# Performance work log

Measured on AMD Instinct MI355X. Metric: run time of the kernel, lower is better.

Reference implementation:

```python
import jax, jax.numpy as jnp
import numpy as np

# LLaMA-style decoder config (shrunken for reference): L layers, hidden D, H heads,
# SwiGLU width F, vocab V, LoRA rank R.
B, S, D, H, F, V, L, R = 2, 512, 1024, 16, 4096, 32000, 2, 16
DH = D // H
LORA_ALPHA = 32.0
EPS = 1e-5
ROPE_THETA = 10000.0


def setup_inputs() -> dict:
    key = jax.random.key(0)
    ks = iter(jax.random.split(key, 40))
    def n(shape, std=0.02):
        return jax.random.normal(next(ks), shape, jnp.float32) * std
    return {
        "input_ids": jax.random.randint(next(ks), (B, S), 0, V),
        "attention_mask": jnp.ones((B, S), jnp.int32),
        "embed": n((V, D)),
        "ln1": jnp.ones((L, D), jnp.float32),
        "ln2": jnp.ones((L, D), jnp.float32),
        "wq": n((L, D, D)), "aq": n((L, D, R)), "bq": n((L, R, D), 0.01),
        "wk": n((L, D, D)), "ak": n((L, D, R)), "bk": n((L, R, D), 0.01),
        "wv": n((L, D, D)), "av": n((L, D, R)), "bv": n((L, R, D), 0.01),
        "wo": n((L, D, D)), "ao": n((L, D, R)), "bo": n((L, R, D), 0.01),
        "wg": n((L, D, F)), "ag": n((L, D, R)), "bg": n((L, R, F), 0.01),
        "wu": n((L, D, F)), "au": n((L, D, R)), "bu": n((L, R, F), 0.01),
        "wd": n((L, F, D)), "ad": n((L, F, R)), "bd": n((L, R, D), 0.01),
        "final_ln": jnp.ones((D,), jnp.float32),
        "lm_head_w": n((D, V)),
        "value_w": n((D, 1)),
        "value_b": jnp.zeros((1,), jnp.float32),
    }


def _rmsnorm(x, w):
    return x * jax.lax.rsqrt(jnp.mean(x * x, axis=-1, keepdims=True) + EPS) * w


def _lin_lora(x, w, a, b):
    # base matmul + low-rank LoRA update scaled by alpha/r (dropout=eval/off)
    return x @ w + ((x @ a) @ b) * (LORA_ALPHA / R)


def _rope_cache(seq_len):
    half = DH // 2
    inv = 1.0 / (ROPE_THETA ** (jnp.arange(half, dtype=jnp.float32) / half))
    ang = jnp.arange(seq_len, dtype=jnp.float32)[:, None] * inv  # [S, half]
    ang = jnp.concatenate([ang, ang], axis=-1)                   # [S, DH]
    return jnp.cos(ang), jnp.sin(ang)


def _apply_rope(x, cos, sin):  # x: [B,S,H,DH]
    h = DH // 2
    rot = jnp.concatenate([-x[..., h:], x[..., :h]], axis=-1)
    return x * cos[None, :, None, :] + rot * sin[None, :, None, :]


def reference(input_ids, attention_mask, embed, ln1, ln2,
              wq, aq, bq, wk, ak, bk, wv, av, bv, wo, ao, bo,
              wg, ag, bg, wu, au, bu, wd, ad, bd,
              final_ln, lm_head_w, value_w, value_b):
    h = embed[input_ids]  # [B,S,D]
    cos, sin = _rope_cache(S)
    causal = jnp.tril(jnp.ones((S, S), bool))
    keep = causal[None, None, :, :] & (attention_mask[:, None, None, :] > 0)
    bias = jnp.where(keep, 0.0, -1e9)  # [B,1,S,S]
    scale = 1.0 / jnp.sqrt(jnp.float32(DH))

    for i in range(L):
        # --- self-attention block ---
        x = _rmsnorm(h, ln1[i])
        q = _lin_lora(x, wq[i], aq[i], bq[i]).reshape(B, S, H, DH)
        k = _lin_lora(x, wk[i], ak[i], bk[i]).reshape(B, S, H, DH)
        v = _lin_lora(x, wv[i], av[i], bv[i]).reshape(B, S, H, DH)
        q = _apply_rope(q, cos, sin)
        k = _apply_rope(k, cos, sin)
        scores = jnp.einsum("bqhd,bkhd->bhqk", q, k) * scale + bias
        attn = jax.nn.softmax(scores, axis=-1)
        o = jnp.einsum("bhqk,bkhd->bqhd", attn, v).reshape(B, S, D)
        h = h + _lin_lora(o, wo[i], ao[i], bo[i])
        # --- SwiGLU MLP block ---
        x = _rmsnorm(h, ln2[i])
        g = jax.nn.silu(_lin_lora(x, wg[i], ag[i], bg[i]))
        u = _lin_lora(x, wu[i], au[i], bu[i])
        h = h + _lin_lora(g * u, wd[i], ad[i], bd[i])

    h = _rmsnorm(h, final_ln)          # HF hidden_states[-1] is post final norm
    logits = h @ lm_head_w             # [B,S,V]
    values = (h @ value_w)[..., 0] + value_b[0]  # [B,S] (squeeze(-1))
    return logits, values
```

## Files before the change

### kernel.cpp

```cpp
#include <hip/hip_runtime.h>
#include <math.h>

constexpr int B = 2, S = 512, D = 1024, H = 16, F = 4096, V = 32000, L = 2, R = 16, DH = 64;
constexpr int BS = B * S;
constexpr float LORA_SCALE = 2.0f;
constexpr float EPS = 1e-5f;
constexpr int RS_QKV = 3 * D;
constexpr int RS_GU  = 2 * F;

typedef __attribute__((ext_vector_type(8))) __bf16 bf16x8;
typedef __attribute__((ext_vector_type(4))) float f32x4;

__device__ __forceinline__ unsigned short f2bf(float f) {
  unsigned u = __builtin_bit_cast(unsigned, f);
  unsigned r = (u + 0x7FFFu + ((u >> 16) & 1u)) >> 16;
  return (unsigned short)r;
}
__device__ __forceinline__ float bf2f(unsigned short us) {
  return __builtin_bit_cast(float, (unsigned)us << 16);
}
__device__ __forceinline__ void load_lds16(const void* g, void* l) {
  __builtin_amdgcn_global_load_lds((const __attribute__((address_space(1))) void*)g,
                                   (__attribute__((address_space(3))) void*)l, 16, 0, 0);
}

struct Ptr3 { const float* p[3]; };

__global__ void rope_cache_kernel(float* __restrict__ cosb, float* __restrict__ sinb) {
  int s = blockIdx.x, j = threadIdx.x;
  float inv = __expf(-(float)j * (9.210340371976184f / 32.0f));
  float ang = (float)s * inv;
  float c = cosf(ang), sn = sinf(ang);
  cosb[s * DH + j] = c;  cosb[s * DH + j + 32] = c;
  sinb[s * DH + j] = sn; sinb[s * DH + j + 32] = sn;
}

__global__ void embed_kernel(const int* __restrict__ ids, const float* __restrict__ emb,
                             float* __restrict__ h) {
  int row = blockIdx.x, t = threadIdx.x;
  int id = ids[row];
  ((float4*)(h + (size_t)row * D))[t] = ((const float4*)(emb + (size_t)id * D))[t];
}

__global__ void rmsnorm_value_kernel(const float* __restrict__ x, const float* __restrict__ w,
                                     const float* __restrict__ vw, const float* __restrict__ vb,
                                     unsigned short* __restrict__ y, float* __restrict__ values) {
  int row = blockIdx.x, t = threadIdx.x;
  int lane = t & 63;
  __shared__ float redw[4];
  __shared__ float redv[4];
  float4 xv = ((const float4*)(x + (size_t)row * D))[t];
  float ss = xv.x * xv.x + xv.y * xv.y + xv.z * xv.z + xv.w * xv.w;
#pragma unroll
  for (int off = 1; off < 64; off <<= 1) ss += __shfl_xor(ss, off);
  if (lane == 0) redw[t >> 6] = ss;
  __syncthreads();
  float rinv = rsqrtf((redw[0] + redw[1] + redw[2] + redw[3]) * (1.0f / D) + EPS);
  float4 wv = ((const float4*)w)[t];
  float4 nx;
  nx.x = xv.x * rinv * wv.x; nx.y = xv.y * rinv * wv.y;
  nx.z = xv.z * rinv * wv.z; nx.w = xv.w * rinv * wv.w;
  ushort4 o;
  o.x = f2bf(nx.x); o.y = f2bf(nx.y); o.z = f2bf(nx.z); o.w = f2bf(nx.w);
  ((ushort4*)(y + (size_t)row * D))[t] = o;
  float4 vv = ((const float4*)vw)[t];
  float vd = nx.x * vv.x + nx.y * vv.y + nx.z * vv.z + nx.w * vv.w;
#pragma unroll
  for (int off = 1; off < 64; off <<= 1) vd += __shfl_xor(vd, off);
  if (lane == 0) redv[t >> 6] = vd;
  __syncthreads();
  if (t == 0) values[row] = redv[0] + redv[1] + redv[2] + redv[3] + vb[0];
}

template <int NA>
__global__ void rms_lora_kernel(const float* __restrict__ hp, const float* __restrict__ w,
                                Ptr3 ap, unsigned short* __restrict__ xbf,
                                unsigned short* __restrict__ t2e) {
  int row = blockIdx.x, t = threadIdx.x;
  int lane = t & 63;
  __shared__ float xs[D];
  __shared__ float red[256];
  __shared__ float redw[4];
  float4 xv = ((const float4*)(hp + (size_t)row * D))[t];
  float ss = xv.x * xv.x + xv.y * xv.y + xv.z * xv.z + xv.w * xv.w;
#pragma unroll
  for (int off = 1; off < 64; off <<= 1) ss += __shfl_xor(ss, off);
  if (lane == 0) redw[t >> 6] = ss;
  __syncthreads();
  float rinv = rsqrtf((redw[0] + redw[1] + redw[2] + redw[3]) * (1.0f / D) + EPS);
  float4 wv = ((const float4*)w)[t];
  float4 nx;
  nx.x = xv.x * rinv * wv.x; nx.y = xv.y * rinv * wv.y;
  nx.z = xv.z * rinv * wv.z; nx.w = xv.w * rinv * wv.w;
  xs[t * 4 + 0] = nx.x; xs[t * 4 + 1] = nx.y; xs[t * 4 + 2] = nx.z; xs[t * 4 + 3] = nx.w;
  ushort4 o;
  o.x = f2bf(nx.x); o.y = f2bf(nx.y); o.z = f2bf(nx.z); o.w = f2bf(nx.w);
  ((ushort4*)(xbf + (size_t)row * D))[t] = o;
  if (t >= NA * 16 && t < 64) t2e[(size_t)row * 64 + t] = 0;
  __syncthreads();
  int n = t & 15, g = t >> 4;
#pragma unroll
  for (int ad = 0; ad < NA; ++ad) {
    const float* a = ap.p[ad];
    float s = 0.0f;
    for (int k = g; k < D; k += 16) s = fmaf(xs[k], a[k * 16 + n], s);
    s += __shfl_xor(s, 16);
    s += __shfl_xor(s, 32);
    if (lane < 16) red[(t >> 6) * 16 + n] = s;
    __syncthreads();
    if (t < 16) t2e[(size_t)row * 64 + ad * 16 + t] =
        f2bf(LORA_SCALE * (red[t] + red[t + 16] + red[t + 32] + red[t + 48]));
    if (ad + 1 < NA) __syncthreads();
  }
}

__global__ void lora_o_kernel(const unsigned short* __restrict__ xb, const float* __restrict__ a,
                              unsigned short* __restrict__ t2e) {
  int row = blockIdx.x, t = threadIdx.x;
  int lane = t & 63;
  __shared__ float xs[D];
  __shared__ float red[64];
  for (int k = t; k < D; k += 256) xs[k] = bf2f(xb[(size_t)row * D + k]);
  if (t >= 16 && t < 64) t2e[(size_t)row * 64 + t] = 0;
  __syncthreads();
  int n = t & 15, g = t >> 4;
  float s = 0.0f;
  for (int k = g; k < D; k += 16) s = fmaf(xs[k], a[k * 16 + n], s);
  s += __shfl_xor(s, 16);
  s += __shfl_xor(s, 32);
  if (lane < 16) red[(t >> 6) * 16 + n] = s;
  __syncthreads();
  if (t < 16) t2e[(size_t)row * 64 + t] =
      f2bf(LORA_SCALE * (red[t] + red[t + 16] + red[t + 32] + red[t + 48]));
}

__global__ void silu_lora_kernel(const unsigned short* __restrict__ gub, const float* __restrict__ a,
                                 unsigned short* __restrict__ gbf, unsigned short* __restrict__ t2e) {
  int row = blockIdx.x, t = threadIdx.x;
  int lane = t & 63;
  __shared__ float xs[F];
  __shared__ float red[64];
#pragma unroll
  for (int i2 = 0; i2 < 2; ++i2) {
    int idx = i2 * 256 + t;
    uint4 gv = ((const uint4*)(gub + (size_t)row * RS_GU))[idx];
    uint4 uv = ((const uint4*)(gub + (size_t)row * RS_GU + F))[idx];
    const unsigned* gw = (const unsigned*)&gv;
    const unsigned* uw = (const unsigned*)&uv;
    unsigned short go[8];
#pragma unroll
    for (int q = 0; q < 4; ++q) {
      float g0 = bf2f((unsigned short)(gw[q] & 0xffff)), g1 = bf2f((unsigned short)(gw[q] >> 16));
      float u0 = bf2f((unsigned short)(uw[q] & 0xffff)), u1 = bf2f((unsigned short)(uw[q] >> 16));
      float r0 = g0 / (1.0f + __expf(-g0)) * u0;
      float r1 = g1 / (1.0f + __expf(-g1)) * u1;
      xs[idx * 8 + q * 2] = r0; xs[idx * 8 + q * 2 + 1] = r1;
      go[q * 2] = f2bf(r0); go[q * 2 + 1] = f2bf(r1);
    }
    *(uint4*)(gbf + (size_t)row * F + idx * 8) = *(const uint4*)go;
  }
  if (t >= 16 && t < 64) t2e[(size_t)row * 64 + t] = 0;
  __syncthreads();
  int n = t & 15, g = t >> 4;
  float s = 0.0f;
  for (int k = g; k < F; k += 16) s = fmaf(xs[k], a[k * 16 + n], s);
  s += __shfl_xor(s, 16);
  s += __shfl_xor(s, 32);
  if (lane < 16) red[(t >> 6) * 16 + n] = s;
  __syncthreads();
  if (t < 16) t2e[(size_t)row * 64 + t] =
      f2bf(LORA_SCALE * (red[t] + red[t + 16] + red[t + 32] + red[t + 48]));
}

struct BD { const float* p0; const float* p1; const float* p2;
            unsigned short* dst; int NA; int logW; int nelem; };
struct BDs { BD d[8]; };
__global__ void bext_many_kernel(BDs da) {
  int gid = blockIdx.x * 256 + threadIdx.x;
  int di = 0;
  while (gid >= da.d[di].nelem) { gid -= da.d[di].nelem; ++di; }
  const BD dd = da.d[di];
  int n = gid >> 6, kk = gid & 63;
  int W = 1 << dd.logW;
  int sel = n >> dd.logW;
  const float* bp = (sel == 0) ? dd.p0 : (sel == 1) ? dd.p1 : dd.p2;
  float v = 0.0f;
  if ((kk >> 4) == sel && sel < dd.NA)
    v = bp[(size_t)(kk & 15) * W + (n & (W - 1))];
  dd.dst[(size_t)n * 64 + kk] = f2bf(v);
}

struct TD { const float* src; unsigned short* dst; int K; int N; int nblk; };
struct TDs { TD d[15]; };
__global__ __launch_bounds__(256) void transpose_many_kernel(TDs da) {
  __shared__ __align__(16) float tile[128 * 128];
  int bid = blockIdx.x;
  int di = 0;
  while (bid >= da.d[di].nblk) { bid -= da.d[di].nblk; ++di; }
  const TD dd = da.d[di];
  int nbx = dd.N >> 7;
  int n0 = (bid % nbx) * 128, k0 = (bid / nbx) * 128;
  int t = threadIdx.x;
#pragma unroll
  for (int i = 0; i < 16; ++i) {
    int s = i * 256 + t;
    int k = s >> 5, cp = s & 31;
    int swz = (k + (k >> 3)) & 31;
    load_lds16(dd.src + (size_t)(k0 + k) * dd.N + n0 + (cp ^ swz) * 4, &tile[s * 4]);
  }
  asm volatile("s_waitcnt vmcnt(0)" ::: "memory");
  __builtin_amdgcn_s_barrier();
#pragma unroll
  for (int j2 = 0; j2 < 8; ++j2) {
    int flat = j2 * 256 + t;
    int n = flat >> 4, kc = flat & 15;
    int n4 = n >> 2;
    unsigned short o8[8];
#pragma unroll
    for (int q = 0; q < 8; ++q) {
      int k = kc * 8 + q;
      int swz = (k + (k >> 3)) & 31;
      o8[q] = f2bf(tile[k * 128 + ((n4 ^ swz) << 2) + (n & 3)]);
    }
    *(uint4*)(dd.dst + (size_t)(n0 + n) * dd.K + k0 + kc * 8) = *(const uint4*)o8;
  }
}

template <int BM, int BN, bool ACC, bool EXT, int OM>
__global__ __launch_bounds__(256) void gemm_bf16_kernel(
    const unsigned short* __restrict__ A, const unsigned short* __restrict__ Bt,
    void* __restrict__ Cp, int M, int N, int K,
    const unsigned short* __restrict__ Ae, const unsigned short* __restrict__ Be,
    const float* __restrict__ cosb, const float* __restrict__ sinb) {
  constexpr int WC = (BM == 64 || BN == 128) ? 2 : 1;
  constexpr int WR = 4 / WC;
  constexpr int RW = BM / WR;
  constexpr int MI = RW / 16;
  constexpr int CN = BN / WC;
  constexpr int NI = CN / 16;
  constexpr int ACH = BM / 32;
  constexpr int BCH = BN / 32;
  constexpr int NLOADS = ACH + BCH;
  __shared__ __align__(16) unsigned short As[2][BM * 64];
  __shared__ __align__(16) unsigned short Bs[2][BN * 64];
  int t = threadIdx.x;
  int lane = t & 63, wave = t >> 6;
  int wr = wave / WC, wc = wave % WC;
  int MT = gridDim.y, NT = gridDim.x;
  int nwg = MT * NT;
  int orig = blockIdx.y * NT + blockIdx.x;
  int qq = nwg >> 3, rr8 = nwg & 7;
  int xcd = orig & 7, pos = orig >> 3;
  int wg = (xcd < rr8) ? (xcd * (qq + 1) + pos) : (rr8 * (qq + 1) + (xcd - rr8) * qq + pos);
  int m0 = (wg % MT) * BM, n0 = (wg / MT) * BN;
  int fr = lane & 15, fq = lane >> 4;
  int xorv = fr & 7;
  f32x4 acc[MI][NI] = {};
  int kIters = K / 64;
  int nIters = EXT ? kIters + 1 : kIters;

  auto STAGE = [&](int it, int buf) {
    bool ext = EXT && (it == kIters);
    int k0 = it * 64;
#pragma unroll
    for (int c = 0; c < ACH; ++c) {
      int i = c * 256 + t;
      int row = i >> 3, c8 = i & 7;
      int sc = (c8 ^ (row & 7)) * 8;
      const unsigned short* src = ext ? (Ae + (size_t)(m0 + row) * 64 + sc)
                                      : (A + (size_t)(m0 + row) * K + k0 + sc);
      load_lds16(src, &As[buf][i * 8]);
    }
#pragma unroll
    for (int c = 0; c < BCH; ++c) {
      int i = c * 256 + t;
      int row = i >> 3, c8 = i & 7;
      int sc = (c8 ^ (row & 7)) * 8;
      const unsigned short* src = ext ? (Be + (size_t)(n0 + row) * 64 + sc)
                                      : (Bt + (size_t)(n0 + row) * K + k0 + sc);
      load_lds16(src, &Bs[buf][i * 8]);
    }
  };

  STAGE(0, 0);
  if (nIters > 1) STAGE(1, 1);
  int cur = 0;
  for (int it = 0; it < nIters; ++it) {
    if (it + 1 < nIters) {
      if constexpr (NLOADS == 8)      asm volatile("s_waitcnt vmcnt(8)" ::: "memory");
      else if constexpr (NLOADS == 6) asm volatile("s_waitcnt vmcnt(6)" ::: "memory");
      else                            asm volatile("s_waitcnt vmcnt(4)" ::: "memory");
    } else {
      asm volatile("s_waitcnt vmcnt(0)" ::: "memory");
    }
    __builtin_amdgcn_s_barrier();
#pragma unroll
    for (int kk = 0; kk < 2; ++kk) {
      bf16x8 af[MI], bfr[NI];
#pragma unroll
      for (int mi = 0; mi < MI; ++mi)
        af[mi] = *(const bf16x8*)(&As[cur][(wr * RW + mi * 16 + fr) * 64 + (((kk * 4 + fq) ^ xorv) << 3)]);
#pragma unroll
      for (int ni = 0; ni < NI; ++ni)
        bfr[ni] = *(const bf16x8*)(&Bs[cur][(wc * CN + ni * 16 + fr) * 64 + (((kk * 4 + fq) ^ xorv) << 3)]);
#pragma unroll
      for (int mi = 0; mi < MI; ++mi)
#pragma unroll
        for (int ni = 0; ni < NI; ++ni)
          acc[mi][ni] = __builtin_amdgcn_mfma_f32_16x16x32_bf16(af[mi], bfr[ni], acc[mi][ni], 0, 0, 0);
    }
    __builtin_amdgcn_s_barrier();
    if (it + 2 < nIters) STAGE(it + 2, cur);
    cur ^= 1;
  }
  if constexpr (OM == 0) {
    float* C = (float*)Cp;
#pragma unroll
    for (int mi = 0; mi < MI; ++mi)
#pragma unroll
      for (int ni = 0; ni < NI; ++ni)
#pragma unroll
        for (int j = 0; j < 4; ++j) {
          int r = m0 + wr * RW + mi * 16 + fq * 4 + j;
          int cl = n0 + wc * CN + ni * 16 + fr;
          size_t idx = (size_t)r * N + cl;
          float v = acc[mi][ni][j];
          C[idx] = ACC ? C[idx] + v : v;
        }
  } else {
    unsigned short* Cb = (unsigned short*)Cp;
#pragma unroll
    for (int mi = 0; mi < MI; ++mi)
#pragma unroll
      for (int j = 0; j < 4; ++j) {
        int r = m0 + wr * RW + mi * 16 + fq * 4 + j;
        if constexpr (OM == 2) {
          int s = r & (S - 1);
#pragma unroll
          for (int ni = 0; ni < 2; ++ni) {
            int cl0 = n0 + wc * CN + ni * 16 + fr;
            int cl1 = cl0 + 32;
            float x0 = acc[mi][ni][j], x1 = acc[mi][ni + 2][j];
            if (cl0 < 2 * D) {
              int dh = cl0 & 63;
              float cz = cosb[s * DH + dh], sz = sinb[s * DH + dh];
              float y0 = x0 * cz - x1 * sz;
              float y1 = x1 * cz + x0 * sz;
              x0 = y0; x1 = y1;
            }
            Cb[(size_t)r * N + cl0] = f2bf(x0);
            Cb[(size_t)r * N + cl1] = f2bf(x1);
          }
        } else {
#pragma unroll
          for (int ni = 0; ni < NI; ++ni) {
            int cl = n0 + wc * CN + ni * 16 + fr;
            Cb[(size_t)r * N + cl] = f2bf(acc[mi][ni][j]);
          }
        }
      }
  }
}

__global__ __launch_bounds__(512) void gemm256_kernel(
    const unsigned short* __restrict__ A, const unsigned short* __restrict__ Bt,
    float* __restrict__ C, int M, int N, int K) {
  __shared__ __align__(16) unsigned short As[2][256 * 64];
  __shared__ __align__(16) unsigned short Bs[2][256 * 64];
  int t = threadIdx.x;
  int lane = t & 63, wave = t >> 6;
  int wr = wave >> 2, wc = wave & 3;
  int MT = gridDim.y, NT = gridDim.x;
  int nwg = MT * NT;
  int orig = blockIdx.y * NT + blockIdx.x;
  int qq = nwg >> 3, rr8 = nwg & 7;
  int xcd = orig & 7, pos = orig >> 3;
  int wg = (xcd < rr8) ? (xcd * (qq + 1) + pos) : (rr8 * (qq + 1) + (xcd - rr8) * qq + pos);
  int m0 = (wg % MT) * 256, n0 = (wg / MT) * 256;
  int fr = lane & 15, fq = lane >> 4;
  int xorv = fr & 7;
  f32x4 acc[8][4] = {};
  int kIters = K / 64;

  auto STAGE = [&](int it, int buf) {
    int k0 = it * 64;
#pragma unroll
    for (int c = 0; c < 4; ++c) {
      int i = c * 512 + t;
      int row = i >> 3, c8 = i & 7;
      int sc = (c8 ^ (row & 7)) * 8;
      load_lds16(A + (size_t)(m0 + row) * K + k0 + sc, &As[buf][i * 8]);
    }
#pragma unroll
    for (int c = 0; c < 4; ++c) {
      int i = c * 512 + t;
      int row = i >> 3, c8 = i & 7;
      int sc = (c8 ^ (row & 7)) * 8;
      load_lds16(Bt + (size_t)(n0 + row) * K + k0 + sc, &Bs[buf][i * 8]);
    }
  };

  STAGE(0, 0);
  if (kIters > 1) STAGE(1, 1);
  int cur = 0;
  for (int it = 0; it < kIters; ++it) {
    if (it + 1 < kIters) asm volatile("s_waitcnt vmcnt(8)" ::: "memory");
    else                 asm volatile("s_waitcnt vmcnt(0)" ::: "memory");
    __builtin_amdgcn_s_barrier();
    __builtin_amdgcn_s_setprio(1);
#pragma unroll
    for (int kk = 0; kk < 2; ++kk) {
      bf16x8 af[8], bfr[4];
#pragma unroll
      for (int mi = 0; mi < 8; ++mi)
        af[mi] = *(const bf16x8*)(&As[cur][(wr * 128 + mi * 16 + fr) * 64 + (((kk * 4 + fq) ^ xorv) << 3)]);
#pragma unroll
      for (int ni = 0; ni < 4; ++ni)
        bfr[ni] = *(const bf16x8*)(&Bs[cur][(wc * 64 + ni * 16 + fr) * 64 + (((kk * 4 + fq) ^ xorv) << 3)]);
#pragma unroll
      for (int mi = 0; mi < 8; ++mi)
#pragma unroll
        for (int ni = 0; ni < 4; ++ni)
          acc[mi][ni] = __builtin_amdgcn_mfma_f32_16x16x32_bf16(af[mi], bfr[ni], acc[mi][ni], 0, 0, 0);
    }
    __builtin_amdgcn_s_setprio(0);
    __builtin_amdgcn_s_barrier();
    if (it + 2 < kIters) STAGE(it + 2, cur);
    cur ^= 1;
  }
#pragma unroll
  for (int mi = 0; mi < 8; ++mi)
#pragma unroll
    for (int ni = 0; ni < 4; ++ni)
#pragma unroll
      for (int j = 0; j < 4; ++j) {
        int r = m0 + wr * 128 + mi * 16 + fq * 4 + j;
        int cl = n0 + wc * 64 + ni * 16 + fr;
        C[(size_t)r * N + cl] = acc[mi][ni][j];
      }
}

__global__ __launch_bounds__(256) void attn_mfma_kernel(
    const unsigned short* __restrict__ qkvb, const int* __restrict__ amask,
    unsigned short* __restrict__ o) {
  __shared__ unsigned short Qs[64 * 72];
  __shared__ unsigned short Ks[64 * 72];
  __shared__ unsigned short Vt[64 * 72];
  __shared__ unsigned short Ps[4][16 * 72];
  __shared__ float msk[64];
  int bid = blockIdx.x;
  int qt = bid & 7, hh = (bid >> 3) & (H - 1), b = bid >> 7;
  int t = threadIdx.x;
  int lane = t & 63, w = t >> 6;
  int fr = lane & 15, fq = lane >> 4;
  size_t rowbase = (size_t)b * S;
  int q0 = qt * 64;
  const float scale = 0.125f;
#pragma unroll
  for (int c = 0; c < 2; ++c) {
    int i = c * 256 + t;
    int row = i >> 3, ch = i & 7;
    *(uint4*)(Qs + row * 72 + ch * 8) =
        *(const uint4*)(qkvb + (rowbase + q0 + row) * RS_QKV + hh * DH + ch * 8);
  }
  f32x4 oacc[4] = {};
  float m_old[4] = {-1e30f, -1e30f, -1e30f, -1e30f};
  float l[4] = {};
  int qbase = q0 + w * 16;
  for (int kt = 0; kt <= qt; ++kt) {
    int kk0 = kt * 64;
#pragma unroll
    for (int c = 0; c < 2; ++c) {
      int i = c * 256 + t;
      int row = i >> 3, ch = i & 7;
      uint4 kv = *(const uint4*)(qkvb + (rowbase + kk0 + row) * RS_QKV + D + hh * DH + ch * 8);
      *(uint4*)(Ks + row * 72 + ch * 8) = kv;
    }
#pragma unroll
    for (int c = 0; c < 2; ++c) {
      int idx = c * 256 + t;
      int rp = idx >> 4, dg = idx & 15;
      const unsigned short* vsrc = qkvb + (rowbase + kk0 + rp * 2) * RS_QKV + 2 * D + hh * DH + dg * 4;
      uint2 lo = *(const uint2*)vsrc;
      uint2 hi = *(const uint2*)(vsrc + RS_QKV);
      const unsigned short* ls = (const unsigned short*)&lo;
      const unsigned short* hs = (const unsigned short*)&hi;
#pragma unroll
      for (int q = 0; q < 4; ++q) {
        unsigned pk = (unsigned)ls[q] | ((unsigned)hs[q] << 16);
        *(unsigned*)(Vt + (dg * 4 + q) * 72 + rp * 2) = pk;
      }
    }
    if (t < 64) msk[t] = (amask[b * S + kk0 + t] > 0) ? 0.0f : -1e9f;
    __syncthreads();
    bf16x8 aq[2];
    aq[0] = *(const bf16x8*)(Qs + (w * 16 + fr) * 72 + fq * 8);
    aq[1] = *(const bf16x8*)(Qs + (w * 16 + fr) * 72 + 32 + fq * 8);
    f32x4 sacc[4];
#pragma unroll
    for (int ct = 0; ct < 4; ++ct) {
      bf16x8 bk0 = *(const bf16x8*)(Ks + (ct * 16 + fr) * 72 + fq * 8);
      bf16x8 bk1 = *(const bf16x8*)(Ks + (ct * 16 + fr) * 72 + 32 + fq * 8);
      f32x4 z = {};
      z = __builtin_amdgcn_mfma_f32_16x16x32_bf16(aq[0], bk0, z, 0, 0, 0);
      sacc[ct] = __builtin_amdgcn_mfma_f32_16x16x32_bf16(aq[1], bk1, z, 0, 0, 0);
    }
    float sv[4][4];
#pragma unroll
    for (int ct = 0; ct < 4; ++ct) {
      int kg = kk0 + ct * 16 + fr;
      float mk = msk[ct * 16 + fr];
#pragma unroll
      for (int j = 0; j < 4; ++j) {
        int qg = qbase + fq * 4 + j;
        float s = sacc[ct][j] * scale + mk;
        sv[ct][j] = (kg > qg) ? -1e9f : s;
      }
    }
    float mnew[4], f[4], rsum[4];
#pragma unroll
    for (int j = 0; j < 4; ++j) {
      float mt = fmaxf(fmaxf(sv[0][j], sv[1][j]), fmaxf(sv[2][j], sv[3][j]));
      for (int off = 1; off < 16; off <<= 1) mt = fmaxf(mt, __shfl_xor(mt, off));
      mnew[j] = fmaxf(m_old[j], mt);
      f[j] = __expf(m_old[j] - mnew[j]);
      float rs = 0.0f;
#pragma unroll
      for (int ct = 0; ct < 4; ++ct) {
        float e = __expf(sv[ct][j] - mnew[j]);
        sv[ct][j] = e;
        rs += e;
      }
      for (int off = 1; off < 16; off <<= 1) rs += __shfl_xor(rs, off);
      rsum[j] = rs;
      l[j] = l[j] * f[j] + rsum[j];
      m_old[j] = mnew[j];
#pragma unroll
      for (int dt = 0; dt < 4; ++dt) oacc[dt][j] *= f[j];
    }
#pragma unroll
    for (int ct = 0; ct < 4; ++ct)
#pragma unroll
      for (int j = 0; j < 4; ++j)
        Ps[w][(fq * 4 + j) * 72 + ct * 16 + fr] = f2bf(sv[ct][j]);
    __syncthreads();
    bf16x8 pa[2];
    pa[0] = *(const bf16x8*)(&Ps[w][fr * 72 + fq * 8]);
    pa[1] = *(const bf16x8*)(&Ps[w][fr * 72 + 32 + fq * 8]);
#pragma unroll
    for (int dt = 0; dt < 4; ++dt) {
      bf16x8 vb0 = *(const bf16x8*)(Vt + (dt * 16 + fr) * 72 + fq * 8);
      bf16x8 vb1 = *(const bf16x8*)(Vt + (dt * 16 + fr) * 72 + 32 + fq * 8);
      oacc[dt] = __builtin_amdgcn_mfma_f32_16x16x32_bf16(pa[0], vb0, oacc[dt], 0, 0, 0);
      oacc[dt] = __builtin_amdgcn_mfma_f32_16x16x32_bf16(pa[1], vb1, oacc[dt], 0, 0, 0);
    }
    __syncthreads();
  }
#pragma unroll
  for (int j = 0; j < 4; ++j) {
    float rinv = 1.0f / l[j];
    int qrow = qbase + fq * 4 + j;
#pragma unroll
    for (int dt = 0; dt < 4; ++dt)
      o[(rowbase + qrow) * D + hh * DH + dt * 16 + fr] = f2bf(oacc[dt][j] * rinv);
  }
}

extern "C" void kernel_launch(void* const* d_in, const int* in_sizes, int n_in,
                              void* d_out, int out_size, void* d_ws, size_t ws_size,
                              hipStream_t stream) {
  const int*   ids     = (const int*)d_in[0];
  const int*   amask   = (const int*)d_in[1];
  const float* emb     = (const float*)d_in[2];
  const float* ln1     = (const float*)d_in[3];
  const float* ln2     = (const float*)d_in[4];
  const float* wq = (const float*)d_in[5],  *aq = (const float*)d_in[6],  *bq = (const float*)d_in[7];
  const float* wk = (const float*)d_in[8],  *ak = (const float*)d_in[9],  *bk = (const float*)d_in[10];
  const float* wv = (const float*)d_in[11], *av = (const float*)d_in[12], *bv = (const float*)d_in[13];
  const float* wo = (const float*)d_in[14], *ao = (const float*)d_in[15], *bo = (const float*)d_in[16];
  const float* wg = (const float*)d_in[17], *ag = (const float*)d_in[18], *bg = (const float*)d_in[19];
  const float* wu = (const float*)d_in[20], *au = (const float*)d_in[21], *bu = (const float*)d_in[22];
  const float* wd = (const float*)d_in[23], *ad = (const float*)d_in[24], *bd = (const float*)d_in[25];
  const float* final_ln  = (const float*)d_in[26];
  const float* lm_head_w = (const float*)d_in[27];
  const float* value_w   = (const float*)d_in[28];
  const float* value_b   = (const float*)d_in[29];

  float* out    = (float*)d_out;
  float* logits = out;
  float* values = out + (size_t)BS * V;

  float* Wf = (float*)d_ws;
  float* cosb = Wf; Wf += S * DH;
  float* sinb = Wf; Wf += S * DH;
  float* h    = Wf; Wf += (size_t)BS * D;
  unsigned short* Wb = (unsigned short*)Wf;
  unsigned short* x_bf  = Wb; Wb += (size_t)BS * D;
  unsigned short* t2e   = Wb; Wb += (size_t)BS * 64;
  unsigned short* qg    = Wb; Wb += (size_t)BS * F;
  unsigned short* gu_bf = Wb; Wb += (size_t)BS * RS_GU;
  unsigned short* wqkvT = Wb; Wb += (size_t)L * 3 * D * D;
  unsigned short* woT   = Wb; Wb += (size_t)L * D * D;
  unsigned short* wguT  = Wb; Wb += (size_t)L * 2 * D * F;
  unsigned short* wdT   = Wb; Wb += (size_t)L * F * D;
  unsigned short* lmT   = Wb; Wb += (size_t)D * V;
  unsigned short* beQKV = Wb; Wb += (size_t)L * 3 * D * 64;
  unsigned short* beO   = Wb; Wb += (size_t)L * D * 64;
  unsigned short* beGU  = Wb; Wb += (size_t)L * 2 * F * 64;
  unsigned short* beD   = Wb; Wb += (size_t)L * D * 64;
  unsigned short* qkv_bf = qg;
  unsigned short* gbf    = qg;
  unsigned short* obf    = gu_bf;

  TDs td; int tblocks = 0; int di = 0;
  auto addT = [&](const float* s, unsigned short* dp, int K_, int N_) {
    td.d[di] = {s, dp, K_, N_, (K_ / 128) * (N_ / 128)};
    tblocks += td.d[di].nblk; ++di;
  };
  for (int l = 0; l < L; ++l) {
    size_t DD = (size_t)D * D, DF = (size_t)D * F;
    addT(wq + l * DD, wqkvT + (size_t)l * 3 * DD, D, D);
    addT(wk + l * DD, wqkvT + (size_t)l * 3 * DD + DD, D, D);
    addT(wv + l * DD, wqkvT + (size_t)l * 3 * DD + 2 * DD, D, D);
    addT(wo + l * DD, woT + l * DD, D, D);
    addT(wg + l * DF, wguT + (size_t)l * 2 * DF, D, F);
    addT(wu + l * DF, wguT + (size_t)l * 2 * DF + DF, D, F);
    addT(wd + l * DF, wdT + l * DF, F, D);
  }
  addT(lm_head_w, lmT, D, V);
  transpose_many_kernel<<<dim3(tblocks), 256, 0, stream>>>(td);

  BDs bd2; int belems = 0; di = 0;
  auto addB = [&](const float* p0, const float* p1, const float* p2,
                  unsigned short* dst, int NA, int logW, int N_) {
    bd2.d[di] = {p0, p1, p2, dst, NA, logW, N_ * 64};
    belems += N_ * 64; ++di;
  };
  for (int l = 0; l < L; ++l) {
    size_t oRD = (size_t)l * R * D, oRF = (size_t)l * R * F;
    addB(bq + oRD, bk + oRD, bv + oRD, beQKV + (size_t)l * 3 * D * 64, 3, 10, 3 * D);
    addB(bo + oRD, nullptr, nullptr,   beO   + (size_t)l * D * 64,     1, 10, D);
    addB(bg + oRF, bu + oRF, nullptr,  beGU  + (size_t)l * 2 * F * 64, 2, 12, 2 * F);
    addB(bd + oRD, nullptr, nullptr,   beD   + (size_t)l * D * 64,     1, 10, D);
  }
  bext_many_kernel<<<dim3(belems / 256), 256, 0, stream>>>(bd2);

  rope_cache_kernel<<<dim3(S), dim3(32), 0, stream>>>(cosb, sinb);
  embed_kernel<<<dim3(BS), dim3(256), 0, stream>>>(ids, emb, h);

  for (int l = 0; l < L; ++l) {
    size_t DD = (size_t)D * D, DF = (size_t)D * F;
    size_t oDR = (size_t)l * D * R, oFR = (size_t)l * F * R;

    { Ptr3 ap = {{aq + oDR, ak + oDR, av + oDR}};
      rms_lora_kernel<3><<<dim3(BS), 256, 0, stream>>>(h, ln1 + (size_t)l * D, ap, x_bf, t2e); }
    gemm_bf16_kernel<64, 128, false, true, 2><<<dim3(3 * D / 128, BS / 64), 256, 0, stream>>>(
        x_bf, wqkvT + (size_t)l * 3 * DD, qkv_bf, BS, 3 * D, D,
        t2e, beQKV + (size_t)l * 3 * D * 64, cosb, sinb);

    attn_mfma_kernel<<<dim3(B * H * (S / 64)), 256, 0, stream>>>(qkv_bf, amask, obf);

    lora_o_kernel<<<dim3(BS), 256, 0, stream>>>(obf, ao + oDR, t2e);
    gemm_bf16_kernel<64, 64, true, true, 0><<<dim3(D / 64, BS / 64), 256, 0, stream>>>(
        obf, woT + l * DD, h, BS, D, D, t2e, beO + (size_t)l * D * 64, nullptr, nullptr);

    { Ptr3 ap = {{ag + oDR, au + oDR, nullptr}};
      rms_lora_kernel<2><<<dim3(BS), 256, 0, stream>>>(h, ln2 + (size_t)l * D, ap, x_bf, t2e); }
    gemm_bf16_kernel<128, 128, false, true, 1><<<dim3(2 * F / 128, BS / 128), 256, 0, stream>>>(
        x_bf, wguT + (size_t)l * 2 * DF, gu_bf, BS, 2 * F, D,
        t2e, beGU + (size_t)l * 2 * F * 64, nullptr, nullptr);

    silu_lora_kernel<<<dim3(BS), 256, 0, stream>>>(gu_bf, ad + oFR, gbf, t2e);

    gemm_bf16_kernel<64, 64, true, true, 0><<<dim3(D / 64, BS / 64), 256, 0, stream>>>(
        gbf, wdT + l * DF, h, BS, D, F, t2e, beD + (size_t)l * D * 64, nullptr, nullptr);
  }

  rmsnorm_value_kernel<<<dim3(BS), 256, 0, stream>>>(h, final_ln, value_w, value_b, x_bf, values);
  gemm256_kernel<<<dim3(V / 256, BS / 256), 512, 0, stream>>>(x_bf, lmT, logits, BS, V, D);
}
```

Baseline: 956.1 us.

## Fuse lm_head fp32-to-bf16 conversion into logits GEMM and shrink transpose tiles

Result: faster. 911.4 us (-4.7%).

```diff
diff --git a/kernel.cpp b/kernel.cpp
--- a/kernel.cpp
+++ b/kernel.cpp
@@ -191,36 +191,35 @@
 }
 
 struct TD { const float* src; unsigned short* dst; int K; int N; int nblk; };
-struct TDs { TD d[15]; };
+struct TDs { TD d[14]; };
 __global__ __launch_bounds__(256) void transpose_many_kernel(TDs da) {
-  __shared__ __align__(16) float tile[128 * 128];
+  __shared__ __align__(16) float tile[128 * 64];
   int bid = blockIdx.x;
   int di = 0;
   while (bid >= da.d[di].nblk) { bid -= da.d[di].nblk; ++di; }
   const TD dd = da.d[di];
-  int nbx = dd.N >> 7;
-  int n0 = (bid % nbx) * 128, k0 = (bid / nbx) * 128;
+  int nbx = dd.N >> 6;
+  int n0 = (bid % nbx) * 64, k0 = (bid / nbx) * 128;
   int t = threadIdx.x;
 #pragma unroll
-  for (int i = 0; i < 16; ++i) {
+  for (int i = 0; i < 8; ++i) {
     int s = i * 256 + t;
-    int k = s >> 5, cp = s & 31;
-    int swz = (k + (k >> 3)) & 31;
-    load_lds16(dd.src + (size_t)(k0 + k) * dd.N + n0 + (cp ^ swz) * 4, &tile[s * 4]);
+    int k = s >> 4, cp = s & 15;
+    int c = cp ^ (k >> 3);
+    load_lds16(dd.src + (size_t)(k0 + k) * dd.N + n0 + c * 4, &tile[s * 4]);
   }
   asm volatile("s_waitcnt vmcnt(0)" ::: "memory");
   __builtin_amdgcn_s_barrier();
 #pragma unroll
-  for (int j2 = 0; j2 < 8; ++j2) {
+  for (int j2 = 0; j2 < 4; ++j2) {
     int flat = j2 * 256 + t;
     int n = flat >> 4, kc = flat & 15;
-    int n4 = n >> 2;
+    int cs = ((n >> 2) ^ kc) << 2;
     unsigned short o8[8];
 #pragma unroll
     for (int q = 0; q < 8; ++q) {
       int k = kc * 8 + q;
-      int swz = (k + (k >> 3)) & 31;
-      o8[q] = f2bf(tile[k * 128 + ((n4 ^ swz) << 2) + (n & 3)]);
+      o8[q] = f2bf(tile[k * 64 + cs + (n & 3)]);
     }
     *(uint4*)(dd.dst + (size_t)(n0 + n) * dd.K + k0 + kc * 8) = *(const uint4*)o8;
   }
@@ -362,11 +361,11 @@
   }
 }
 
-__global__ __launch_bounds__(512) void gemm256_kernel(
-    const unsigned short* __restrict__ A, const unsigned short* __restrict__ Bt,
+__global__ __launch_bounds__(512) void gemm256f_kernel(
+    const unsigned short* __restrict__ A, const float* __restrict__ Bsrc,
     float* __restrict__ C, int M, int N, int K) {
-  __shared__ __align__(16) unsigned short As[2][256 * 64];
-  __shared__ __align__(16) unsigned short Bs[2][256 * 64];
+  __shared__ __align__(16) unsigned short As[256 * 64];
+  __shared__ __align__(16) char BsB[256 * 144];
   int t = threadIdx.x;
   int lane = t & 63, wave = t >> 6;
   int wr = wave >> 2, wc = wave & 3;
@@ -381,42 +380,72 @@
   int xorv = fr & 7;
   f32x4 acc[8][4] = {};
   int kIters = K / 64;
-
-  auto STAGE = [&](int it, int buf) {
+  float4 blo[4], bhi[4];
+  int kq = wave;
+  int n4 = lane;
+
+  auto B_LOAD = [&](int it) {
+    int k0 = it * 64;
+#pragma unroll
+    for (int i = 0; i < 4; ++i) {
+      int kb = i * 16 + kq * 2;
+      blo[i] = *(const float4*)(Bsrc + (size_t)(k0 + kb) * N + n0 + n4 * 4);
+      bhi[i] = *(const float4*)(Bsrc + (size_t)(k0 + kb + 1) * N + n0 + n4 * 4);
+    }
+  };
+  auto B_WRITE = [&]() {
+#pragma unroll
+    for (int i = 0; i < 4; ++i) {
+      int kb = i * 16 + kq * 2;
+      int ch0 = kb >> 3, koff = kb & 7;
+      const float* lo = (const float*)&blo[i];
+      const float* hi = (const float*)&bhi[i];
+#pragma unroll
+      for (int j = 0; j < 4; ++j) {
+        int n = n4 * 4 + j;
+        int swz = (n & 7) ^ ((n >> 3) & 7);
+        unsigned pk = (unsigned)f2bf(lo[j]) | ((unsigned)f2bf(hi[j]) << 16);
+        *(unsigned*)(BsB + n * 144 + ((ch0 ^ swz) << 4) + koff * 2) = pk;
+      }
+    }
+  };
+  auto A_STAGE = [&](int it) {
     int k0 = it * 64;
 #pragma unroll
     for (int c = 0; c < 4; ++c) {
       int i = c * 512 + t;
       int row = i >> 3, c8 = i & 7;
       int sc = (c8 ^ (row & 7)) * 8;
-      load_lds16(A + (size_t)(m0 + row) * K + k0 + sc, &As[buf][i * 8]);
-    }
-#pragma unroll
-    for (int c = 0; c < 4; ++c) {
-      int i = c * 512 + t;
-      int row = i >> 3, c8 = i & 7;
-      int sc = (c8 ^ (row & 7)) * 8;
-      load_lds16(Bt + (size_t)(n0 + row) * K + k0 + sc, &Bs[buf][i * 8]);
+      load_lds16(A + (size_t)(m0 + row) * K + k0 + sc, &As[i * 8]);
     }
   };
 
-  STAGE(0, 0);
-  if (kIters > 1) STAGE(1, 1);
-  int cur = 0;
+  B_LOAD(0);
   for (int it = 0; it < kIters; ++it) {
-    if (it + 1 < kIters) asm volatile("s_waitcnt vmcnt(8)" ::: "memory");
-    else                 asm volatile("s_waitcnt vmcnt(0)" ::: "memory");
-    __builtin_amdgcn_s_barrier();
+    __syncthreads();
+    A_STAGE(it);
+    asm volatile("s_waitcnt vmcnt(4)" ::: "memory");
+    B_WRITE();
+    if (it + 1 < kIters) {
+      B_LOAD(it + 1);
+      asm volatile("s_waitcnt vmcnt(8)" ::: "memory");
+    } else {
+      asm volatile("s_waitcnt vmcnt(0)" ::: "memory");
+    }
+    __syncthreads();
     __builtin_amdgcn_s_setprio(1);
 #pragma unroll
     for (int kk = 0; kk < 2; ++kk) {
       bf16x8 af[8], bfr[4];
 #pragma unroll
       for (int mi = 0; mi < 8; ++mi)
-        af[mi] = *(const bf16x8*)(&As[cur][(wr * 128 + mi * 16 + fr) * 64 + (((kk * 4 + fq) ^ xorv) << 3)]);
-#pragma unroll
-      for (int ni = 0; ni < 4; ++ni)
-        bfr[ni] = *(const bf16x8*)(&Bs[cur][(wc * 64 + ni * 16 + fr) * 64 + (((kk * 4 + fq) ^ xorv) << 3)]);
+        af[mi] = *(const bf16x8*)(&As[(wr * 128 + mi * 16 + fr) * 64 + (((kk * 4 + fq) ^ xorv) << 3)]);
+#pragma unroll
+      for (int ni = 0; ni < 4; ++ni) {
+        int n = wc * 64 + ni * 16 + fr;
+        int swz = (n & 7) ^ ((n >> 3) & 7);
+        bfr[ni] = *(const bf16x8*)(BsB + n * 144 + (((kk * 4 + fq) ^ swz) << 4));
+      }
 #pragma unroll
       for (int mi = 0; mi < 8; ++mi)
 #pragma unroll
@@ -424,9 +453,6 @@
           acc[mi][ni] = __builtin_amdgcn_mfma_f32_16x16x32_bf16(af[mi], bfr[ni], acc[mi][ni], 0, 0, 0);
     }
     __builtin_amdgcn_s_setprio(0);
-    __builtin_amdgcn_s_barrier();
-    if (it + 2 < kIters) STAGE(it + 2, cur);
-    cur ^= 1;
   }
 #pragma unroll
   for (int mi = 0; mi < 8; ++mi)
@@ -603,7 +629,6 @@
   unsigned short* woT   = Wb; Wb += (size_t)L * D * D;
   unsigned short* wguT  = Wb; Wb += (size_t)L * 2 * D * F;
   unsigned short* wdT   = Wb; Wb += (size_t)L * F * D;
-  unsigned short* lmT   = Wb; Wb += (size_t)D * V;
   unsigned short* beQKV = Wb; Wb += (size_t)L * 3 * D * 64;
   unsigned short* beO   = Wb; Wb += (size_t)L * D * 64;
   unsigned short* beGU  = Wb; Wb += (size_t)L * 2 * F * 64;
@@ -614,7 +639,7 @@
 
   TDs td; int tblocks = 0; int di = 0;
   auto addT = [&](const float* s, unsigned short* dp, int K_, int N_) {
-    td.d[di] = {s, dp, K_, N_, (K_ / 128) * (N_ / 128)};
+    td.d[di] = {s, dp, K_, N_, (K_ / 128) * (N_ / 64)};
     tblocks += td.d[di].nblk; ++di;
   };
   for (int l = 0; l < L; ++l) {
@@ -627,7 +652,6 @@
     addT(wu + l * DF, wguT + (size_t)l * 2 * DF + DF, D, F);
     addT(wd + l * DF, wdT + l * DF, F, D);
   }
-  addT(lm_head_w, lmT, D, V);
   transpose_many_kernel<<<dim3(tblocks), 256, 0, stream>>>(td);
 
   BDs bd2; int belems = 0; di = 0;
@@ -677,5 +701,5 @@
   }
 
   rmsnorm_value_kernel<<<dim3(BS), 256, 0, stream>>>(h, final_ln, value_w, value_b, x_bf, values);
-  gemm256_kernel<<<dim3(V / 256, BS / 256), 512, 0, stream>>>(x_bf, lmT, logits, BS, V, D);
-}
+  gemm256f_kernel<<<dim3(V / 256, BS / 256), 512, 0, stream>>>(x_bf, lm_head_w, logits, BS, V, D);
+}
```
